# Performance work log

Measured on AMD Instinct MI355X. Metric: run time of the kernel, lower is better.

Reference implementation:

```python
import jax, jax.numpy as jnp
import numpy as np

TEMPERATURE = 0.5
B, D = 4096, 256

def setup_inputs() -> dict:
    key = jax.random.key(0)
    k1, k2 = jax.random.split(key)
    z_i = jax.random.normal(k1, (B, D), dtype=jnp.float32)
    z_j = jax.random.normal(k2, (B, D), dtype=jnp.float32)
    return {"z_i": z_i, "z_j": z_j}

def reference(z_i, z_j):
    # NT-Xent loss (SimCLR). Cosine similarity of L2-normalized rows == dot product.
    b = z_i.shape[0]
    n = 2 * b
    zi = z_i / jnp.linalg.norm(z_i, axis=1, keepdims=True)
    zj = z_j / jnp.linalg.norm(z_j, axis=1, keepdims=True)
    z = jnp.concatenate([zi, zj], axis=0)            # [N, D]
    sim = jnp.matmul(z, z.T)                          # [N, N] cosine-sim matrix
    # positives: sim(i, i+b) and sim(i+b, i)
    pos = jnp.concatenate([jnp.diagonal(sim, offset=b), jnp.diagonal(sim, offset=-b)])  # [N]
    logits = sim / TEMPERATURE
    # Cross-entropy with the positive as the target class over {pos} U negatives.
    # The candidate set per row is all j != i (the positive j = partner(i) is included,
    # only the self-similarity diagonal is excluded) -> mask diagonal with -inf.
    neg_inf = jnp.asarray(-jnp.inf, dtype=logits.dtype)
    masked = jnp.where(jnp.eye(n, dtype=bool), neg_inf, logits)
    lse = jax.nn.logsumexp(masked, axis=1)            # [N]
    loss = jnp.sum(lse - pos / TEMPERATURE) / n
    return loss
```

## Files before the change

kernel.cpp:

```cpp
#include <hip/hip_runtime.h>
#include <hip/hip_bf16.h>


constexpr int BB = 4096;
constexpr int NN = 8192;
constexpr int DD = 256;
constexpr int TILE = 256;
constexpr int NT = NN / TILE;
constexpr int NBLK = NT * (NT + 1) / 2;
constexpr int CSTEPS = TILE / 32;

typedef _Float16 half4v __attribute__((ext_vector_type(4)));
typedef _Float16 half8v __attribute__((ext_vector_type(8)));
typedef float floatx16 __attribute__((ext_vector_type(16)));

__global__ __launch_bounds__(256) void nt_normalize(
    const float* __restrict__ zi, const float* __restrict__ zj,
    _Float16* __restrict__ Z, float* __restrict__ posPartial,
    float* __restrict__ rowsum)
{
    const int lane = threadIdx.x & 63;
    const int wave = threadIdx.x >> 6;
    const int i = blockIdx.x * 4 + wave;

    if (blockIdx.x < 32) rowsum[blockIdx.x * 256 + threadIdx.x] = 0.f;

    const float4 a = ((const float4*)(zi + (size_t)i * DD))[lane];
    const float4 b = ((const float4*)(zj + (size_t)i * DD))[lane];

    float ssi = a.x*a.x + a.y*a.y + a.z*a.z + a.w*a.w;
    float ssj = b.x*b.x + b.y*b.y + b.z*b.z + b.w*b.w;
    float dd  = a.x*b.x + a.y*b.y + a.z*b.z + a.w*b.w;
#pragma unroll
    for (int off = 32; off > 0; off >>= 1) {
        ssi += __shfl_xor(ssi, off);
        ssj += __shfl_xor(ssj, off);
        dd  += __shfl_xor(dd,  off);
    }
    const float invi = rsqrtf(ssi);
    const float invj = rsqrtf(ssj);

    half4v ha, hb;
    ha.x = (_Float16)(a.x * invi); ha.y = (_Float16)(a.y * invi);
    ha.z = (_Float16)(a.z * invi); ha.w = (_Float16)(a.w * invi);
    hb.x = (_Float16)(b.x * invj); hb.y = (_Float16)(b.y * invj);
    hb.z = (_Float16)(b.z * invj); hb.w = (_Float16)(b.w * invj);

    ((half4v*)(Z + (size_t)i * DD))[lane]        = ha;
    ((half4v*)(Z + (size_t)(BB + i) * DD))[lane] = hb;

    __shared__ float ps[4];
    if (lane == 0) ps[wave] = dd * invi * invj;
    __syncthreads();
    if (threadIdx.x == 0)
        posPartial[blockIdx.x] = ps[0] + ps[1] + ps[2] + ps[3];
}

__device__ __forceinline__ float half_sums(float x) {
    int t;
    t = __builtin_amdgcn_update_dpp(0, __builtin_bit_cast(int, x), 0x111, 0xf, 0xf, false);
    x += __builtin_bit_cast(float, t);
    t = __builtin_amdgcn_update_dpp(0, __builtin_bit_cast(int, x), 0x112, 0xf, 0xf, false);
    x += __builtin_bit_cast(float, t);
    t = __builtin_amdgcn_update_dpp(0, __builtin_bit_cast(int, x), 0x114, 0xf, 0xf, false);
    x += __builtin_bit_cast(float, t);
    t = __builtin_amdgcn_update_dpp(0, __builtin_bit_cast(int, x), 0x118, 0xf, 0xf, false);
    x += __builtin_bit_cast(float, t);
    t = __builtin_amdgcn_update_dpp(0, __builtin_bit_cast(int, x), 0x142, 0xa, 0xf, false);
    x += __builtin_bit_cast(float, t);
    return x;
}

__global__ __launch_bounds__(256, 2) void nt_simexp(
    const _Float16* __restrict__ Z, float* __restrict__ rowsum)
{
    __shared__ _Float16 lds[2][32 * DD];
    __shared__ float colacc[TILE];

    int bid = (blockIdx.x & 7) * (NBLK / 8) + (blockIdx.x >> 3);

    int rt = 0, rem = bid;
    while (rem >= NT - rt) { rem -= NT - rt; ++rt; }
    const int ct = rt + rem;
    const bool diag = (rt == ct);

    const int tid = threadIdx.x;
    const int wave = tid >> 6;
    const int lane = tid & 63;
    const int lm = lane & 31;
    const int lh = lane >> 5;

    const int rbase = rt * TILE + wave * 64;
    const int cbase0 = ct * TILE;

    colacc[tid] = 0.f;

    half8v bfrag[2][16];
#pragma unroll
    for (int b = 0; b < 2; ++b) {
        const _Float16* rowp = Z + (size_t)(rbase + b * 32 + lm) * DD + lh * 8;
#pragma unroll
        for (int s = 0; s < 16; ++s)
            bfrag[b][s] = *(const half8v*)(rowp + s * 16);
    }

    const int g_c0 = tid >> 5;
    const int g_kc = tid & 31;

    half8v pre[4];
    auto loadTile = [&](int crow0) {
#pragma unroll
        for (int it = 0; it < 4; ++it) {
            const int c = g_c0 + it * 8;
            pre[it] = *(const half8v*)(Z + (size_t)(crow0 + c) * DD + g_kc * 8);
        }
    };
    auto storeTile = [&](int bi) {
#pragma unroll
        for (int it = 0; it < 4; ++it) {
            const int c = g_c0 + it * 8;
            *(half8v*)(&lds[bi][c * DD + (g_kc ^ (c & 7)) * 8]) = pre[it];
        }
    };

    float ea0 = 0.f, ea1 = 0.f;
    const float KEXP = 2.0f * 1.44269504088896340736f;

    loadTile(cbase0);
    storeTile(0);

    for (int cs = 0; cs < CSTEPS; ++cs) {
        __syncthreads();
        if (cs + 1 < CSTEPS) loadTile(cbase0 + (cs + 1) * 32);

        const _Float16* buf = lds[cs & 1];
        floatx16 c0, c1;
#pragma unroll
        for (int r = 0; r < 16; ++r) { c0[r] = 0.f; c1[r] = 0.f; }

#pragma unroll
        for (int s = 0; s < 16; ++s) {
            const int phys = (2 * s + lh) ^ (lm & 7);
            half8v af = *(const half8v*)(&buf[lm * DD + phys * 8]);
            c0 = __builtin_amdgcn_mfma_f32_32x32x16_f16(af, bfrag[0][s], c0, 0, 0, 0);
            c1 = __builtin_amdgcn_mfma_f32_32x32x16_f16(af, bfrag[1][s], c1, 0, 0, 0);
        }

        if (!diag) {
#pragma unroll
            for (int r = 0; r < 16; ++r) {
                float e0 = __builtin_amdgcn_exp2f(c0[r] * KEXP);
                float e1 = __builtin_amdgcn_exp2f(c1[r] * KEXP);
                ea0 += e0; ea1 += e1;
                float s2 = half_sums(e0 + e1);
                if (lm == 31) {
                    const int cidx = cs * 32 + (r & 3) + 8 * (r >> 2) + 4 * lh;
                    atomicAdd(&colacc[cidx], s2);
                }
            }
        } else {
            const bool m0 = (cs == 2 * wave);
            const bool m1 = (cs == 2 * wave + 1);
#pragma unroll
            for (int r = 0; r < 16; ++r) {
                const int mrow = (r & 3) + 8 * (r >> 2) + 4 * lh;
                float e0 = __builtin_amdgcn_exp2f(c0[r] * KEXP);
                float e1 = __builtin_amdgcn_exp2f(c1[r] * KEXP);
                if (m0 && (mrow == lm)) e0 = 0.f;
                if (m1 && (mrow == lm)) e1 = 0.f;
                ea0 += e0; ea1 += e1;
            }
        }

        if (cs + 1 < CSTEPS) storeTile((cs + 1) & 1);
    }

    ea0 += __shfl_xor(ea0, 32);
    ea1 += __shfl_xor(ea1, 32);
    if (lane < 32) {
        atomicAdd(&rowsum[rbase + lm], ea0);
        atomicAdd(&rowsum[rbase + 32 + lm], ea1);
    }

    if (!diag) {
        __syncthreads();
        atomicAdd(&rowsum[cbase0 + tid], colacc[tid]);
    }
}

__global__ __launch_bounds__(256) void nt_finalize(
    const float* __restrict__ rowsum, const float* __restrict__ posPartial,
    float* __restrict__ out)
{
    const int tid = threadIdx.x;
    float acc = 0.f;
#pragma unroll
    for (int it = 0; it < NN / 256; ++it)
        acc += __builtin_amdgcn_logf(rowsum[tid + it * 256]);
    float pacc = 0.f;
#pragma unroll
    for (int it = 0; it < 4; ++it)
        pacc += posPartial[tid + it * 256];

#pragma unroll
    for (int off = 32; off > 0; off >>= 1) {
        acc  += __shfl_xor(acc,  off);
        pacc += __shfl_xor(pacc, off);
    }
    __shared__ float sa[4], sp[4];
    const int wave = tid >> 6;
    if ((tid & 63) == 0) { sa[wave] = acc; sp[wave] = pacc; }
    __syncthreads();
    if (tid == 0) {
        const float lntot = (sa[0] + sa[1] + sa[2] + sa[3]) * 0.6931471805599453f;
        const float ptot  = sp[0] + sp[1] + sp[2] + sp[3];
        out[0] = (lntot - 4.0f * ptot) * (1.0f / (float)NN);
    }
}

extern "C" void kernel_launch(void* const* d_in, const int* in_sizes, int n_in,
                              void* d_out, int out_size, void* d_ws, size_t ws_size,
                              hipStream_t stream) {
    const float* zi = (const float*)d_in[0];
    const float* zj = (const float*)d_in[1];
    float* out = (float*)d_out;

    _Float16* Z = (_Float16*)d_ws;
    float* rowsum = (float*)((char*)d_ws + (size_t)NN * DD * 2);
    float* posPartial = rowsum + NN;

    nt_normalize<<<BB / 4, 256, 0, stream>>>(zi, zj, Z, posPartial, rowsum);
    nt_simexp<<<NBLK, 256, 0, stream>>>((const _Float16*)Z, rowsum);
    nt_finalize<<<1, 256, 0, stream>>>(rowsum, posPartial, out);
}
```

Before: 99.89 us.

## Retile similarity kernel to 128x128 tiles with K-chunked direct global-to-LDS loads

Replaces the 256-row tile with register-resident row fragments by 128x128 tiles. Both operands are staged in 64-wide K chunks into LDS through global_load_lds, and each wave computes a 64x64 sub-block with four MFMA accumulators. Occupancy rises to 4 blocks per CU and the number of triangular blocks grows, which spreads the work more evenly. In exchange, each chunk is single-buffered with a full vmcnt wait and two barriers, so load and compute no longer overlap, and more blocks mean more atomics on rowsum.

New measurement: 91.30 us. -8.6%, faster.

```diff
diff --git a/kernel.cpp b/kernel.cpp
--- a/kernel.cpp
+++ b/kernel.cpp
@@ -5,10 +5,11 @@
 constexpr int BB = 4096;
 constexpr int NN = 8192;
 constexpr int DD = 256;
-constexpr int TILE = 256;
-constexpr int NT = NN / TILE;
+constexpr int TS = 128;
+constexpr int NT = NN / TS;
 constexpr int NBLK = NT * (NT + 1) / 2;
-constexpr int CSTEPS = TILE / 32;
+constexpr int KCH = 64;
+constexpr int NCH = DD / KCH;
 
 typedef _Float16 half4v __attribute__((ext_vector_type(4)));
 typedef _Float16 half8v __attribute__((ext_vector_type(8)));
@@ -71,13 +72,14 @@
     return x;
 }
 
-__global__ __launch_bounds__(256, 2) void nt_simexp(
+__global__ __launch_bounds__(256, 4) void nt_simexp(
     const _Float16* __restrict__ Z, float* __restrict__ rowsum)
 {
-    __shared__ _Float16 lds[2][32 * DD];
-    __shared__ float colacc[TILE];
-
-    int bid = (blockIdx.x & 7) * (NBLK / 8) + (blockIdx.x >> 3);
+    __shared__ _Float16 As[TS * KCH];
+    __shared__ _Float16 Bs[TS * KCH];
+    __shared__ float colacc[TS];
+
+    const int bid = (blockIdx.x & 7) * (NBLK / 8) + (blockIdx.x >> 3);
 
     int rt = 0, rem = bid;
     while (rem >= NT - rt) { rem -= NT - rt; ++rt; }
@@ -89,102 +91,90 @@
     const int lane = tid & 63;
     const int lm = lane & 31;
     const int lh = lane >> 5;
-
-    const int rbase = rt * TILE + wave * 64;
-    const int cbase0 = ct * TILE;
-
-    colacc[tid] = 0.f;
-
-    half8v bfrag[2][16];
-#pragma unroll
-    for (int b = 0; b < 2; ++b) {
-        const _Float16* rowp = Z + (size_t)(rbase + b * 32 + lm) * DD + lh * 8;
-#pragma unroll
-        for (int s = 0; s < 16; ++s)
-            bfrag[b][s] = *(const half8v*)(rowp + s * 16);
-    }
-
-    const int g_c0 = tid >> 5;
-    const int g_kc = tid & 31;
-
-    half8v pre[4];
-    auto loadTile = [&](int crow0) {
-#pragma unroll
-        for (int it = 0; it < 4; ++it) {
-            const int c = g_c0 + it * 8;
-            pre[it] = *(const half8v*)(Z + (size_t)(crow0 + c) * DD + g_kc * 8);
+    const int wr = wave >> 1;
+    const int wc = wave & 1;
+
+    const int rbase = rt * TS;
+    const int cbase = ct * TS;
+
+    if (tid < TS) colacc[tid] = 0.f;
+
+    const int st_row = (lane >> 3);
+    const int st_sg  = (lane & 7) ^ (lane >> 3);
+    auto stage = [&](const _Float16* srcBase, _Float16* ldsBase, int ch) {
+#pragma unroll
+        for (int j = 0; j < 4; ++j) {
+            const int c = wave * 4 + j;
+            const _Float16* g = srcBase + (size_t)(8 * c + st_row) * DD
+                                        + ch * KCH + st_sg * 8;
+            __builtin_amdgcn_global_load_lds(
+                (const __attribute__((address_space(1))) unsigned int*)g,
+                (__attribute__((address_space(3))) unsigned int*)(ldsBase + c * 512),
+                16, 0, 0);
         }
     };
-    auto storeTile = [&](int bi) {
-#pragma unroll
-        for (int it = 0; it < 4; ++it) {
-            const int c = g_c0 + it * 8;
-            *(half8v*)(&lds[bi][c * DD + (g_kc ^ (c & 7)) * 8]) = pre[it];
+
+    floatx16 a00, a01, a10, a11;
+#pragma unroll
+    for (int r = 0; r < 16; ++r) { a00[r] = 0.f; a01[r] = 0.f; a10[r] = 0.f; a11[r] = 0.f; }
+
+    const _Float16* Ar = Z + (size_t)rbase * DD;
+    const _Float16* Br = Z + (size_t)cbase * DD;
+
+    for (int ch = 0; ch < NCH; ++ch) {
+        __syncthreads();
+        stage(Ar, As, ch);
+        stage(Br, Bs, ch);
+        asm volatile("s_waitcnt vmcnt(0)" ::: "memory");
+        __syncthreads();
+
+#pragma unroll
+        for (int s = 0; s < 4; ++s) {
+            const int pg = 2 * s + lh;
+            const int ph = (pg ^ (lm & 7)) * 8;
+            half8v fa0 = *(const half8v*)&As[(wr * 64 + lm) * KCH + ph];
+            half8v fa1 = *(const half8v*)&As[(wr * 64 + 32 + lm) * KCH + ph];
+            half8v fb0 = *(const half8v*)&Bs[(wc * 64 + lm) * KCH + ph];
+            half8v fb1 = *(const half8v*)&Bs[(wc * 64 + 32 + lm) * KCH + ph];
+            a00 = __builtin_amdgcn_mfma_f32_32x32x16_f16(fa0, fb0, a00, 0, 0, 0);
+            a01 = __builtin_amdgcn_mfma_f32_32x32x16_f16(fa0, fb1, a01, 0, 0, 0);
+            a10 = __builtin_amdgcn_mfma_f32_32x32x16_f16(fa1, fb0, a10, 0, 0, 0);
+            a11 = __builtin_amdgcn_mfma_f32_32x32x16_f16(fa1, fb1, a11, 0, 0, 0);
         }
-    };
-
-    float ea0 = 0.f, ea1 = 0.f;
+    }
+
     const float KEXP = 2.0f * 1.44269504088896340736f;
-
-    loadTile(cbase0);
-    storeTile(0);
-
-    for (int cs = 0; cs < CSTEPS; ++cs) {
-        __syncthreads();
-        if (cs + 1 < CSTEPS) loadTile(cbase0 + (cs + 1) * 32);
-
-        const _Float16* buf = lds[cs & 1];
-        floatx16 c0, c1;
-#pragma unroll
-        for (int r = 0; r < 16; ++r) { c0[r] = 0.f; c1[r] = 0.f; }
-
-#pragma unroll
-        for (int s = 0; s < 16; ++s) {
-            const int phys = (2 * s + lh) ^ (lm & 7);
-            half8v af = *(const half8v*)(&buf[lm * DD + phys * 8]);
-            c0 = __builtin_amdgcn_mfma_f32_32x32x16_f16(af, bfrag[0][s], c0, 0, 0, 0);
-            c1 = __builtin_amdgcn_mfma_f32_32x32x16_f16(af, bfrag[1][s], c1, 0, 0, 0);
-        }
-
-        if (!diag) {
-#pragma unroll
-            for (int r = 0; r < 16; ++r) {
-                float e0 = __builtin_amdgcn_exp2f(c0[r] * KEXP);
-                float e1 = __builtin_amdgcn_exp2f(c1[r] * KEXP);
-                ea0 += e0; ea1 += e1;
+    float eb0 = 0.f, eb1 = 0.f;
+#pragma unroll
+    for (int tr = 0; tr < 2; ++tr) {
+#pragma unroll
+        for (int r = 0; r < 16; ++r) {
+            const int mrow = (r & 3) + 8 * (r >> 2) + 4 * lh;
+            float e0 = __builtin_amdgcn_exp2f((tr ? a10[r] : a00[r]) * KEXP);
+            float e1 = __builtin_amdgcn_exp2f((tr ? a11[r] : a01[r]) * KEXP);
+            if (diag && (wr == wc) && (mrow == lm)) {
+                if (tr == 0) e0 = 0.f; else e1 = 0.f;
+            }
+            if (diag && (wr == wc) && (mrow == lm) && (tr == 1)) e0 = e0;
+            eb0 += e0; eb1 += e1;
+            if (!diag) {
                 float s2 = half_sums(e0 + e1);
-                if (lm == 31) {
-                    const int cidx = cs * 32 + (r & 3) + 8 * (r >> 2) + 4 * lh;
-                    atomicAdd(&colacc[cidx], s2);
-                }
-            }
-        } else {
-            const bool m0 = (cs == 2 * wave);
-            const bool m1 = (cs == 2 * wave + 1);
-#pragma unroll
-            for (int r = 0; r < 16; ++r) {
-                const int mrow = (r & 3) + 8 * (r >> 2) + 4 * lh;
-                float e0 = __builtin_amdgcn_exp2f(c0[r] * KEXP);
-                float e1 = __builtin_amdgcn_exp2f(c1[r] * KEXP);
-                if (m0 && (mrow == lm)) e0 = 0.f;
-                if (m1 && (mrow == lm)) e1 = 0.f;
-                ea0 += e0; ea1 += e1;
+                if (lm == 31)
+                    atomicAdd(&colacc[wr * 64 + tr * 32 + mrow], s2);
             }
         }
-
-        if (cs + 1 < CSTEPS) storeTile((cs + 1) & 1);
-    }
-
-    ea0 += __shfl_xor(ea0, 32);
-    ea1 += __shfl_xor(ea1, 32);
+    }
+
+
+    eb0 += __shfl_xor(eb0, 32);
+    eb1 += __shfl_xor(eb1, 32);
     if (lane < 32) {
-        atomicAdd(&rowsum[rbase + lm], ea0);
-        atomicAdd(&rowsum[rbase + 32 + lm], ea1);
-    }
-
+        atomicAdd(&rowsum[cbase + wc * 64 + lm], eb0);
+        atomicAdd(&rowsum[cbase + wc * 64 + 32 + lm], eb1);
+    }
     if (!diag) {
         __syncthreads();
-        atomicAdd(&rowsum[cbase0 + tid], colacc[tid]);
+        if (tid < TS) atomicAdd(&rowsum[rbase + tid], colacc[tid]);
     }
 }
 
```
